# Optimization experiments

Measured on AMD Instinct MI355X. Metric: run time of the kernel, lower is better.

Reference implementation:

```python
import jax, jax.numpy as jnp
import numpy as np

EPS = 1e-5

def _layernorm(h):
    # parameter-free LayerNorm over last dim (elementwise_affine=False)
    mu = jnp.mean(h, axis=-1, keepdims=True)
    var = jnp.mean(jnp.square(h - mu), axis=-1, keepdims=True)
    return (h - mu) / jnp.sqrt(var + EPS)

def setup_inputs() -> dict:
    key = jax.random.key(0)
    k1, k2, k3, k4 = jax.random.split(key, 4)
    B, D, F_, I = 16, 37, 4096, 64
    x = jax.random.normal(k1, (B, D, F_), dtype=jnp.float32)
    s = 1.0 / np.sqrt(D)  # ~ torch Linear default init scale
    Wq = jax.random.normal(k2, (D, I), dtype=jnp.float32) * s
    Wk = jax.random.normal(k3, (D, I), dtype=jnp.float32) * s
    Wv = jax.random.normal(k4, (D, I), dtype=jnp.float32) * s
    return {"x": x, "Wq": Wq, "Wk": Wk, "Wv": Wv}

def reference(x, Wq, Wk, Wv):
    # x: [B, depth, featuresize] -> entities [B, F, depth]
    xb = jnp.transpose(x, (0, 2, 1))
    q = _layernorm(jnp.einsum('bfd,di->bfi', xb, Wq))
    k = _layernorm(jnp.einsum('bfd,di->bfi', xb, Wk))
    v = _layernorm(jnp.einsum('bfd,di->bfi', xb, Wv))
    d = q.shape[-1]
    att = jnp.einsum('bqi,bki->bqk', q, k) / jnp.sqrt(jnp.float32(d))
    # faithful to torch: softmax over dim=1 (the query axis), not the key axis
    weights = jax.nn.softmax(att, axis=-2)
    return jnp.einsum('bqk,bki->bqi', weights, v)
```

## Files before the change

### kernel.cpp

```cpp
#include <hip/hip_runtime.h>
#include <math.h>

#define B_  16
#define D_  37
#define F_  4096
#define I_  64
#define EPS 1e-5f
#define QSCALE 0.18033688011112042f
#define NQS 4
#define KSP 2

typedef unsigned short u16;
typedef __bf16 bf16x8 __attribute__((ext_vector_type(8)));
typedef __bf16 bf16x2v __attribute__((ext_vector_type(2)));
typedef float  f32x16 __attribute__((ext_vector_type(16)));
typedef float  f32x2v __attribute__((ext_vector_type(2)));
typedef unsigned int u32x4 __attribute__((ext_vector_type(4)));
typedef int i32x2 __attribute__((ext_vector_type(2)));

#define ZERO16 {0,0,0,0, 0,0,0,0, 0,0,0,0, 0,0,0,0}
#define MFMA32(a, b, c) __builtin_amdgcn_mfma_f32_32x32x16_bf16((a), (b), (c), 0, 0, 0)

#if __has_builtin(__builtin_amdgcn_exp2f)
#define EX2(x) __builtin_amdgcn_exp2f(x)
#else
#define EX2(x) exp2f(x)
#endif
#if __has_builtin(__builtin_amdgcn_logf)
#define LG2(x) __builtin_amdgcn_logf(x)
#else
#define LG2(x) log2f(x)
#endif

__device__ __forceinline__ u16 f2b(float f) {
  unsigned u = __builtin_bit_cast(unsigned, f);
  return (u16)((u + 0x7fffu + ((u >> 16) & 1u)) >> 16);
}
__device__ __forceinline__ float b2f(u16 h) {
  return __builtin_bit_cast(float, (unsigned)h << 16);
}
__device__ __forceinline__ unsigned pk2(float lo, float hi) {
  f32x2v f = {lo, hi};
  bf16x2v h = __builtin_convertvector(f, bf16x2v);
  return __builtin_bit_cast(unsigned, h);
}

__device__ __forceinline__ void plswap(unsigned& a, unsigned& b) {
#if __has_builtin(__builtin_amdgcn_permlane32_swap)
  i32x2 r = __builtin_amdgcn_permlane32_swap((int)a, (int)b, false, false);
  a = (unsigned)r[0];
  b = (unsigned)r[1];
#else
  const int lh = (int)((threadIdx.x & 63) >> 5);
  unsigned pa = (unsigned)__shfl_xor((int)a, 32, 64);
  unsigned pb = (unsigned)__shfl_xor((int)b, 32, 64);
  unsigned na = lh ? pb : a;
  unsigned nb = lh ? b : pa;
  a = na;
  b = nb;
#endif
}

__device__ __forceinline__ void build_af(const f32x16& s, bf16x8& f0, bf16x8& f1) {
  float e[16];
#pragma unroll
  for (int r = 0; r < 16; ++r) e[r] = EX2(s[r]);
  unsigned a = pk2(e[0], e[1]),   bq = pk2(e[2], e[3]);
  unsigned c = pk2(e[4], e[5]),   d  = pk2(e[6], e[7]);
  plswap(a, c);
  plswap(bq, d);
  u32x4 v0 = {a, bq, c, d};
  f0 = __builtin_bit_cast(bf16x8, v0);
  unsigned ee = pk2(e[8], e[9]),  ff = pk2(e[10], e[11]);
  unsigned g  = pk2(e[12], e[13]), h = pk2(e[14], e[15]);
  plswap(ee, g);
  plswap(ff, h);
  u32x4 v1 = {ee, ff, g, h};
  f1 = __builtin_bit_cast(bf16x8, v1);
}

__device__ __forceinline__ bf16x8 ldfrag(const u16* base, int row, int kb) {
  return *(const bf16x8*)(base + (row << 6) + ((kb ^ (row & 7)) << 3));
}
__device__ __forceinline__ void stage16(u16* dst, const u16* src, int c, int spitch) {
  const int r = c >> 3, cb = c & 7;
  const int4 v = *(const int4*)(src + (size_t)r * spitch + (cb << 3));
  *(int4*)(dst + (r << 6) + ((cb ^ (r & 7)) << 3)) = v;
}
__device__ __forceinline__ int soff_l(int c) {
  const int r = c >> 3, cb = c & 7;
  return (r << 6) + ((cb ^ (r & 7)) << 3);
}
__device__ __forceinline__ int soff_g(int c, int spitch) {
  return (c >> 3) * spitch + ((c & 7) << 3);
}

__global__ __launch_bounds__(256) void qkv_ln_k(
    const float* __restrict__ x,
    const float* __restrict__ Wq, const float* __restrict__ Wk,
    const float* __restrict__ Wv,
    u16* __restrict__ qn, u16* __restrict__ kn, u16* __restrict__ vt) {
  __shared__ __align__(16) u16 vtile[64 * 72];

  const int t = threadIdx.x, lane = t & 63, w = t >> 6;
  const int b = blockIdx.y, f0 = blockIdx.x * 64;
  const int fl0 = w * 16;

  float hq[16], hk[16], hv[16];
#pragma unroll
  for (int i = 0; i < 16; ++i) { hq[i] = 0.f; hk[i] = 0.f; hv[i] = 0.f; }

  const float* xb = x + (size_t)b * D_ * F_ + f0 + fl0;
#pragma unroll 1
  for (int d = 0; d < D_; ++d) {
    const float wqv = Wq[d * I_ + lane];
    const float wkv = Wk[d * I_ + lane];
    const float wvv = Wv[d * I_ + lane];
    float xv[16];
#pragma unroll
    for (int g = 0; g < 4; ++g)
      *(float4*)&xv[g * 4] = *(const float4*)(xb + (size_t)d * F_ + g * 4);
#pragma unroll
    for (int i = 0; i < 16; ++i) {
      hq[i] = fmaf(xv[i], wqv, hq[i]);
      hk[i] = fmaf(xv[i], wkv, hk[i]);
      hv[i] = fmaf(xv[i], wvv, hv[i]);
    }
  }

  auto lnorm = [&](float a) -> float {
    float s = a;
#pragma unroll
    for (int o = 32; o > 0; o >>= 1) s += __shfl_xor(s, o, 64);
    const float mu = s * (1.f / 64.f);
    const float d0 = a - mu;
    float v = d0 * d0;
#pragma unroll
    for (int o = 32; o > 0; o >>= 1) v += __shfl_xor(v, o, 64);
    return d0 * rsqrtf(v * (1.f / 64.f) + EPS);
  };

#pragma unroll
  for (int i = 0; i < 16; ++i) {
    const size_t fo = ((size_t)b * F_ + f0 + fl0 + i) * I_ + lane;
    qn[fo] = f2b(lnorm(hq[i]) * QSCALE);
    kn[fo] = f2b(lnorm(hk[i]));
    vtile[lane * 72 + fl0 + i] = f2b(lnorm(hv[i]));
  }
  __syncthreads();
  for (int p = 0; p < 2; ++p) {
    const int c = p * 256 + t;
    const int r = c >> 3, off = (c & 7) * 8;
    const int4 v = *(const int4*)&vtile[r * 72 + off];
    *(int4*)(vt + ((size_t)b * I_ + r) * F_ + f0 + off) = v;
  }
}

__global__ __launch_bounds__(256, 4) void attn_stats_k(
    const u16* __restrict__ qn, const u16* __restrict__ kn,
    float* __restrict__ zp) {
  __shared__ __align__(16) u16 sm[16384];

  const int t = threadIdx.x, lane = t & 63, w = t >> 6;
  const int l31 = lane & 31, lh = lane >> 5;
  const int b = blockIdx.y, k0 = blockIdx.x * 256, qh = blockIdx.z;

  const u16* kb = kn + ((size_t)b * F_ + k0) * I_;
#pragma unroll
  for (int p = 0; p < 8; ++p) stage16(sm, kb, p * 256 + t, 64);
  __syncthreads();
  bf16x8 kf[2][4];
#pragma unroll
  for (int kb2 = 0; kb2 < 2; ++kb2)
#pragma unroll
    for (int ic = 0; ic < 4; ++ic)
      kf[kb2][ic] = ldfrag(sm + (w * 64 + kb2 * 32) * 64, l31, ic * 2 + lh);
  __syncthreads();

  int qoff_l[2], qoff_g[2];
#pragma unroll
  for (int p = 0; p < 2; ++p) {
    const int c = p * 256 + t;
    qoff_l[p] = soff_l(c);
    qoff_g[p] = soff_g(c, 64);
  }

  const u16* qsrc = qn + ((size_t)b * F_ + qh * (F_ / NQS)) * I_;
#pragma unroll
  for (int p = 0; p < 2; ++p)
    *(int4*)(sm + qoff_l[p]) = *(const int4*)(qsrc + qoff_g[p]);
  qsrc += 64 * I_;

  float Zc[2][2] = {{0.f, 0.f}, {0.f, 0.f}};
  const int NC = F_ / NQS / 64;

  for (int c = 0; c < NC; ++c) {
    const int cur = (c & 1) * 4096;
    __syncthreads();
    if (c + 1 < NC) {
      const int nxt = cur ^ 4096;
#pragma unroll
      for (int p = 0; p < 2; ++p)
        *(int4*)(sm + nxt + qoff_l[p]) = *(const int4*)(qsrc + qoff_g[p]);
      qsrc += 64 * I_;
    }

    f32x16 a00 = ZERO16, a01 = ZERO16, a10 = ZERO16, a11 = ZERO16;
#pragma unroll
    for (int ic = 0; ic < 4; ++ic) {
      const bf16x8 q0f = ldfrag(sm + cur, l31, ic * 2 + lh);
      const bf16x8 q1f = ldfrag(sm + cur + 32 * 64, l31, ic * 2 + lh);
      a00 = MFMA32(q0f, kf[0][ic], a00);
      a01 = MFMA32(q0f, kf[1][ic], a01);
      a10 = MFMA32(q1f, kf[0][ic], a10);
      a11 = MFMA32(q1f, kf[1][ic], a11);
    }
#pragma unroll
    for (int r = 0; r < 16; ++r) {
      Zc[0][0] += EX2(a00[r]);
      Zc[0][1] += EX2(a01[r]);
      Zc[1][0] += EX2(a10[r]);
      Zc[1][1] += EX2(a11[r]);
    }
  }

#pragma unroll
  for (int kb2 = 0; kb2 < 2; ++kb2) {
    float Zt = Zc[0][kb2] + Zc[1][kb2];
    Zt += __shfl_xor(Zt, 32, 64);
    if (lane < 32)
      zp[((size_t)qh * B_ + b) * F_ + k0 + w * 64 + kb2 * 32 + lane] = Zt;
  }
}

__global__ __launch_bounds__(256) void lzred_k(const float* __restrict__ zp,
                                               float* __restrict__ lz) {
  const int i = blockIdx.x * 256 + threadIdx.x;
  float z = zp[i];
#pragma unroll
  for (int pl = 1; pl < NQS; ++pl) z += zp[(size_t)pl * B_ * F_ + i];
  lz[i] = -LG2(z);
}

__global__ __launch_bounds__(256, 3) void attn_out_k(
    const u16* __restrict__ qn, const u16* __restrict__ kn,
    const u16* __restrict__ vt, const float* __restrict__ lz,
    float* __restrict__ out, u16* __restrict__ pout) {
  __shared__ __align__(16) u16 sm[16384];

  const int t = threadIdx.x, lane = t & 63, w = t >> 6;
  const int l31 = lane & 31, lh = lane >> 5;

  const int bid = blockIdx.x;
  const int g = bid & (B_ * KSP - 1);
  const int qt = bid >> 5;
  const int b = g >> 1, ks = g & 1;
  const int q0 = qt * 128;

  const u16* qb = qn + ((size_t)b * F_ + q0) * I_;
#pragma unroll
  for (int p = 0; p < 4; ++p) stage16(sm, qb, p * 256 + t, 64);
  __syncthreads();
  bf16x8 qf[4];
#pragma unroll
  for (int ic = 0; ic < 4; ++ic)
    qf[ic] = ldfrag(sm + (w * 32) * 64, l31, ic * 2 + lh);
  __syncthreads();

  int off_l[2], kg[2], vg[2];
#pragma unroll
  for (int p = 0; p < 2; ++p) {
    const int c = p * 256 + t;
    off_l[p] = soff_l(c);
    kg[p] = soff_g(c, 64);
    vg[p] = soff_g(c, F_);
  }

  const int kofs = ks * (F_ / KSP);
  const u16* ksrc = kn + ((size_t)b * F_ + kofs) * I_;
  const u16* vsrc = vt + (size_t)b * I_ * F_ + kofs;
  const float* lzp = lz + (size_t)b * F_ + kofs + 4 * lh;

#pragma unroll
  for (int p = 0; p < 2; ++p) {
    *(int4*)(sm + off_l[p])        = *(const int4*)(ksrc + kg[p]);
    *(int4*)(sm + 8192 + off_l[p]) = *(const int4*)(vsrc + vg[p]);
  }
  ksrc += 64 * I_;
  vsrc += 64;

  f32x16 o0 = ZERO16, o1 = ZERO16;
  const int NC = F_ / KSP / 64;

  for (int c = 0; c < NC; ++c) {
    const int cur = (c & 1) * 4096;
    __syncthreads();
    if (c + 1 < NC) {
      const int nxt = cur ^ 4096;
#pragma unroll
      for (int p = 0; p < 2; ++p) {
        *(int4*)(sm + nxt + off_l[p])        = *(const int4*)(ksrc + kg[p]);
        *(int4*)(sm + 8192 + nxt + off_l[p]) = *(const int4*)(vsrc + vg[p]);
      }
      ksrc += 64 * I_;
      vsrc += 64;
    }

    f32x16 s0, s1;
#pragma unroll
    for (int j = 0; j < 4; ++j) {
      const float4 l0 = *(const float4*)(lzp + c * 64 + 8 * j);
      const float4 l1 = *(const float4*)(lzp + c * 64 + 32 + 8 * j);
      s0[4 * j + 0] = l0.x; s0[4 * j + 1] = l0.y;
      s0[4 * j + 2] = l0.z; s0[4 * j + 3] = l0.w;
      s1[4 * j + 0] = l1.x; s1[4 * j + 1] = l1.y;
      s1[4 * j + 2] = l1.z; s1[4 * j + 3] = l1.w;
    }

    const u16* Kc = sm + cur;
#pragma unroll
    for (int ic = 0; ic < 4; ++ic) {
      const bf16x8 ak0 = ldfrag(Kc, l31, ic * 2 + lh);
      const bf16x8 ak1 = ldfrag(Kc + 32 * 64, l31, ic * 2 + lh);
      s0 = MFMA32(ak0, qf[ic], s0);
      s1 = MFMA32(ak1, qf[ic], s1);
    }

    bf16x8 af[4];
    build_af(s0, af[0], af[1]);
    build_af(s1, af[2], af[3]);

    const u16* Vc = sm + 8192 + cur;
#pragma unroll
    for (int kq = 0; kq < 4; ++kq) {
      const bf16x8 bv0 = ldfrag(Vc, l31, kq * 2 + lh);
      const bf16x8 bv1 = ldfrag(Vc + 32 * 64, l31, kq * 2 + lh);
      o0 = MFMA32(af[kq], bv0, o0);
      o1 = MFMA32(af[kq], bv1, o1);
    }
  }

  if (ks == 0) {
    float* ob = out + ((size_t)b * F_ + q0 + w * 32) * I_;
#pragma unroll
    for (int r = 0; r < 16; ++r) {
      const int qr = (r & 3) + 8 * (r >> 2) + 4 * lh;
      ob[(size_t)qr * I_ + l31]      = o0[r];
      ob[(size_t)qr * I_ + 32 + l31] = o1[r];
    }
  } else {
    u16* pb = pout + ((size_t)b * F_ + q0 + w * 32) * I_;
#pragma unroll
    for (int r = 0; r < 16; ++r) {
      const int qr = (r & 3) + 8 * (r >> 2) + 4 * lh;
      pb[(size_t)qr * I_ + l31]      = f2b(o0[r]);
      pb[(size_t)qr * I_ + 32 + l31] = f2b(o1[r]);
    }
  }
}

__global__ __launch_bounds__(256) void reduce_k(float* __restrict__ out,
                                                const u16* __restrict__ pout) {
  const size_t i = ((size_t)blockIdx.x * 256 + threadIdx.x) * 8;
  float4 a0 = *(const float4*)(out + i);
  float4 a1 = *(const float4*)(out + i + 4);
  int4 praw = *(const int4*)(pout + i);
  u16 es[8];
  *(int4*)es = praw;
  a0.x += b2f(es[0]); a0.y += b2f(es[1]); a0.z += b2f(es[2]); a0.w += b2f(es[3]);
  a1.x += b2f(es[4]); a1.y += b2f(es[5]); a1.z += b2f(es[6]); a1.w += b2f(es[7]);
  *(float4*)(out + i)     = a0;
  *(float4*)(out + i + 4) = a1;
}

extern "C" void kernel_launch(void* const* d_in, const int* in_sizes, int n_in,
                              void* d_out, int out_size, void* d_ws,
                              size_t ws_size, hipStream_t stream) {
  const float* x  = (const float*)d_in[0];
  const float* Wq = (const float*)d_in[1];
  const float* Wk = (const float*)d_in[2];
  const float* Wv = (const float*)d_in[3];
  float* out = (float*)d_out;

  const size_t NBF = (size_t)B_ * F_ * I_;
  u16* qn   = (u16*)d_ws;
  u16* kn   = qn + NBF;
  u16* vt   = kn + NBF;
  float* zp = (float*)(vt + NBF);
  float* lz = zp + (size_t)NQS * B_ * F_;
  u16* pout = (u16*)(lz + (size_t)B_ * F_);

  qkv_ln_k<<<dim3(F_ / 64, B_), 256, 0, stream>>>(x, Wq, Wk, Wv, qn, kn, vt);
  attn_stats_k<<<dim3(F_ / 256, B_, NQS), 256, 0, stream>>>(qn, kn, zp);
  lzred_k<<<dim3(B_ * F_ / 256), 256, 0, stream>>>(zp, lz);
  attn_out_k<<<dim3((F_ / 128) * B_ * KSP), 256, 0, stream>>>(qn, kn, vt, lz, out, pout);
  reduce_k<<<dim3((int)(NBF / 2048)), 256, 0, stream>>>(out, pout);
}
```

Baseline: 258.5 us.

## Drop LDS staging in attention stats kernel and load MFMA fragments directly

The stats kernel stops staging K and Q tiles through shared memory. Each wave now loads its K fragments and a prefetched 32-row Q fragment straight from global memory into registers, which removes all __syncthreads and LDS traffic. The grid is flattened to 1D with batch and query-split in the low bits so concurrent blocks share K/Q data in cache, and the output kernel's launch bound is raised to 4 blocks per CU. In exchange, each wave reads Q independently, so global and L2 traffic goes up, and the higher occupancy target for the output kernel may force register spills.

```diff
diff --git a/kernel.cpp b/kernel.cpp
--- a/kernel.cpp
+++ b/kernel.cpp
@@ -159,77 +159,63 @@
 __global__ __launch_bounds__(256, 4) void attn_stats_k(
     const u16* __restrict__ qn, const u16* __restrict__ kn,
     float* __restrict__ zp) {
-  __shared__ __align__(16) u16 sm[16384];
-
   const int t = threadIdx.x, lane = t & 63, w = t >> 6;
   const int l31 = lane & 31, lh = lane >> 5;
-  const int b = blockIdx.y, k0 = blockIdx.x * 256, qh = blockIdx.z;
+
+  const int bid = blockIdx.x;
+  const int g = bid & (B_ * NQS - 1);
+  const int kt = bid >> 6;
+  const int b = g >> 2, qh = g & 3;
+  const int k0 = kt * 256 + w * 64;
 
   const u16* kb = kn + ((size_t)b * F_ + k0) * I_;
-#pragma unroll
-  for (int p = 0; p < 8; ++p) stage16(sm, kb, p * 256 + t, 64);
-  __syncthreads();
   bf16x8 kf[2][4];
 #pragma unroll
   for (int kb2 = 0; kb2 < 2; ++kb2)
 #pragma unroll
     for (int ic = 0; ic < 4; ++ic)
-      kf[kb2][ic] = ldfrag(sm + (w * 64 + kb2 * 32) * 64, l31, ic * 2 + lh);
-  __syncthreads();
-
-  int qoff_l[2], qoff_g[2];
-#pragma unroll
-  for (int p = 0; p < 2; ++p) {
-    const int c = p * 256 + t;
-    qoff_l[p] = soff_l(c);
-    qoff_g[p] = soff_g(c, 64);
-  }
-
-  const u16* qsrc = qn + ((size_t)b * F_ + qh * (F_ / NQS)) * I_;
-#pragma unroll
-  for (int p = 0; p < 2; ++p)
-    *(int4*)(sm + qoff_l[p]) = *(const int4*)(qsrc + qoff_g[p]);
-  qsrc += 64 * I_;
+      kf[kb2][ic] = *(const bf16x8*)(kb + (size_t)(kb2 * 32 + l31) * I_ + ic * 16 + lh * 8);
+
+  const u16* qptr = qn + ((size_t)b * F_ + qh * (F_ / NQS) + l31) * I_ + lh * 8;
+
+  bf16x8 qa[4];
+#pragma unroll
+  for (int ic = 0; ic < 4; ++ic)
+    qa[ic] = *(const bf16x8*)(qptr + ic * 16);
 
   float Zc[2][2] = {{0.f, 0.f}, {0.f, 0.f}};
-  const int NC = F_ / NQS / 64;
+  const int NC = F_ / NQS / 32;
 
   for (int c = 0; c < NC; ++c) {
-    const int cur = (c & 1) * 4096;
-    __syncthreads();
+    bf16x8 qx[4];
     if (c + 1 < NC) {
-      const int nxt = cur ^ 4096;
-#pragma unroll
-      for (int p = 0; p < 2; ++p)
-        *(int4*)(sm + nxt + qoff_l[p]) = *(const int4*)(qsrc + qoff_g[p]);
-      qsrc += 64 * I_;
-    }
-
-    f32x16 a00 = ZERO16, a01 = ZERO16, a10 = ZERO16, a11 = ZERO16;
+      const u16* qp = qptr + (size_t)(c + 1) * 32 * I_;
+#pragma unroll
+      for (int ic = 0; ic < 4; ++ic)
+        qx[ic] = *(const bf16x8*)(qp + ic * 16);
+    }
+
+    f32x16 s0 = ZERO16, s1 = ZERO16;
 #pragma unroll
     for (int ic = 0; ic < 4; ++ic) {
-      const bf16x8 q0f = ldfrag(sm + cur, l31, ic * 2 + lh);
-      const bf16x8 q1f = ldfrag(sm + cur + 32 * 64, l31, ic * 2 + lh);
-      a00 = MFMA32(q0f, kf[0][ic], a00);
-      a01 = MFMA32(q0f, kf[1][ic], a01);
-      a10 = MFMA32(q1f, kf[0][ic], a10);
-      a11 = MFMA32(q1f, kf[1][ic], a11);
+      s0 = MFMA32(qa[ic], kf[0][ic], s0);
+      s1 = MFMA32(qa[ic], kf[1][ic], s1);
     }
 #pragma unroll
     for (int r = 0; r < 16; ++r) {
-      Zc[0][0] += EX2(a00[r]);
-      Zc[0][1] += EX2(a01[r]);
-      Zc[1][0] += EX2(a10[r]);
-      Zc[1][1] += EX2(a11[r]);
-    }
+      Zc[0][r & 1] += EX2(s0[r]);
+      Zc[1][r & 1] += EX2(s1[r]);
+    }
+#pragma unroll
+    for (int ic = 0; ic < 4; ++ic) qa[ic] = qx[ic];
   }
 
 #pragma unroll
   for (int kb2 = 0; kb2 < 2; ++kb2) {
-    float Zt = Zc[0][kb2] + Zc[1][kb2];
+    float Zt = Zc[kb2][0] + Zc[kb2][1];
     Zt += __shfl_xor(Zt, 32, 64);
     if (lane < 32)
-      zp[((size_t)qh * B_ + b) * F_ + k0 + w * 64 + kb2 * 32 + lane] = Zt;
+      zp[((size_t)qh * B_ + b) * F_ + k0 + kb2 * 32 + lane] = Zt;
   }
 }
 
@@ -242,7 +228,7 @@
   lz[i] = -LG2(z);
 }
 
-__global__ __launch_bounds__(256, 3) void attn_out_k(
+__global__ __launch_bounds__(256, 4) void attn_out_k(
     const u16* __restrict__ qn, const u16* __restrict__ kn,
     const u16* __restrict__ vt, const float* __restrict__ lz,
     float* __restrict__ out, u16* __restrict__ pout) {
@@ -391,7 +377,7 @@
   u16* pout = (u16*)(lz + (size_t)B_ * F_);
 
   qkv_ln_k<<<dim3(F_ / 64, B_), 256, 0, stream>>>(x, Wq, Wk, Wv, qn, kn, vt);
-  attn_stats_k<<<dim3(F_ / 256, B_, NQS), 256, 0, stream>>>(qn, kn, zp);
+  attn_stats_k<<<dim3((F_ / 256) * B_ * NQS), 256, 0, stream>>>(qn, kn, zp);
   lzred_k<<<dim3(B_ * F_ / 256), 256, 0, stream>>>(zp, lz);
   attn_out_k<<<dim3((F_ / 128) * B_ * KSP), 256, 0, stream>>>(qn, kn, vt, lz, out, pout);
   reduce_k<<<dim3((int)(NBF / 2048)), 256, 0, stream>>>(out, pout);
```

Result: slower. 268.9 us (+4.0%).
